# Kernel tuning notes

Hardware: AMD Instinct MI355X
Metric: run time of the kernel (lower is better)

## Reference

```python
import jax, jax.numpy as jnp
import numpy as np

B, L, H, D, T = 8, 4096, 8, 128, 128  # batch, max_len, kv_heads, head_size, max_new_tokens


def setup_inputs() -> dict:
    key = jax.random.key(0)
    ks = jax.random.split(key, 6)
    return {
        "keys": jax.random.normal(ks[0], (B, L, H, D), dtype=jnp.float32),
        "values": jax.random.normal(ks[1], (B, L, H, D), dtype=jnp.float32),
        "lengths": jax.random.randint(ks[2], (B,), 0, 2048, dtype=jnp.int32),
        "new_keys": jax.random.normal(ks[3], (B, T, H, D), dtype=jnp.float32),
        "new_values": jax.random.normal(ks[4], (B, T, H, D), dtype=jnp.float32),
        "new_lengths": jax.random.randint(ks[5], (B,), 0, T, dtype=jnp.int32),
    }


def reference(keys, values, lengths, new_keys, new_values, new_lengths):
    max_new_tokens = new_values.shape[1]
    max_len = keys.shape[1]
    operands = (keys, values, lengths, new_keys, new_values, new_lengths)

    def specialized_path(ops):
        k, v, l, nk, nv, nl = ops
        batch_size = k.shape[0]
        batch_idx = jnp.arange(batch_size)
        pos_idx = l
        update_vals_k = nk[:, 0]
        update_vals_v = nv[:, 0]
        should_update = (nl == 1)[:, None, None]
        original_vals_k = k[batch_idx, pos_idx]
        original_vals_v = v[batch_idx, pos_idx]
        vals_to_set_k = jnp.where(should_update, update_vals_k, original_vals_k)
        vals_to_set_v = jnp.where(should_update, update_vals_v, original_vals_v)
        updated_k = k.at[batch_idx, pos_idx].set(vals_to_set_k)
        updated_v = v.at[batch_idx, pos_idx].set(vals_to_set_v)
        return (updated_k, updated_v)

    def general_path(ops):
        k, v, l, nk, nv, nl = ops
        batch_size = k.shape[0]
        b_coords, p_coords = jnp.indices((batch_size, max_len))
        lengths_b = l[:, None]
        new_lengths_b = nl[:, None]
        update_mask = (p_coords >= lengths_b) & (p_coords < lengths_b + new_lengths_b)
        source_indices = p_coords - lengths_b
        clipped_source_indices = jnp.clip(source_indices, 0, max_new_tokens - 1)
        values_to_write_k = nk[b_coords, clipped_source_indices]
        values_to_write_v = nv[b_coords, clipped_source_indices]
        broadcast_mask = update_mask[:, :, None, None]
        updated_k = jnp.where(broadcast_mask, values_to_write_k, k)
        updated_v = jnp.where(broadcast_mask, values_to_write_v, v)
        return (updated_k, updated_v)

    is_special_case = jnp.all(new_lengths <= 1)
    updated_keys, updated_values = jax.lax.cond(is_special_case, specialized_path, general_path, operands)
    updated_lengths = lengths + new_lengths
    return (updated_keys, updated_values, updated_lengths)
```

## Files before the change

### kernel.cpp

```cpp
#include <hip/hip_runtime.h>

constexpr int B = 8;
constexpr int L = 4096;
constexpr int H = 8;
constexpr int D = 128;
constexpr int T = 128;

constexpr long long KV_ELEMS = (long long)B * L * H * D;
constexpr size_t KV_BYTES = (size_t)KV_ELEMS * sizeof(float);

__global__ __launch_bounds__(256) void kv_patch(
    const float4* __restrict__ new_keys,
    const float4* __restrict__ new_values,
    const int*    __restrict__ lengths,
    const int*    __restrict__ new_lengths,
    float4* __restrict__ out_k,
    float4* __restrict__ out_v,
    float*  __restrict__ out_len)
{
    const int b = blockIdx.x >> 7;
    const int t = blockIdx.x & (T - 1);

    if (t < new_lengths[b]) {
        const int l = lengths[b];
        const int c = threadIdx.x;
        const long long srci = ((long long)(b * T + t) << 8) + c;
        const long long dsti = ((long long)(b * L + l + t) << 8) + c;
        out_k[dsti] = new_keys[srci];
        out_v[dsti] = new_values[srci];
    }

    if (blockIdx.x == 0 && threadIdx.x < B) {
        const int bb = threadIdx.x;
        out_len[bb] = (float)(lengths[bb] + new_lengths[bb]);
    }
}

extern "C" void kernel_launch(void* const* d_in, const int* in_sizes, int n_in,
                              void* d_out, int out_size, void* d_ws, size_t ws_size,
                              hipStream_t stream)
{
    const void* keys        = d_in[0];
    const void* values      = d_in[1];
    const int*  lengths     = (const int*)d_in[2];
    const float4* new_keys  = (const float4*)d_in[3];
    const float4* new_values= (const float4*)d_in[4];
    const int*  new_lengths = (const int*)d_in[5];

    float*  out     = (float*)d_out;
    float4* out_k   = (float4*)out;
    float4* out_v   = (float4*)(out + KV_ELEMS);
    float*  out_len = out + 2 * KV_ELEMS;

    hipMemcpyAsync(out_k, keys,   KV_BYTES, hipMemcpyDeviceToDevice, stream);
    hipMemcpyAsync(out_v, values, KV_BYTES, hipMemcpyDeviceToDevice, stream);

    kv_patch<<<B * T, 256, 0, stream>>>(new_keys, new_values, lengths, new_lengths,
                                        out_k, out_v, out_len);
}
```

Measured before the change: 110.4 us.

## Fuse KV copy and patch into one nontemporal grid-stride kernel

Replaces two device-to-device memcpys plus a patch kernel with a single kernel that streams keys and values, substitutes new tokens in the update window, and writes outputs with nontemporal loads and stores. This is meant to remove the extra launches and the separate rewrite pass over patched rows. The loop is not unrolled and each thread keeps only one float4 per tensor in flight, which may limit memory parallelism compared with the tuned copy engine path.

```diff
diff --git a/kernel.cpp b/kernel.cpp
--- a/kernel.cpp
+++ b/kernel.cpp
@@ -7,27 +7,47 @@
 constexpr int T = 128;
 
 constexpr long long KV_ELEMS = (long long)B * L * H * D;
-constexpr size_t KV_BYTES = (size_t)KV_ELEMS * sizeof(float);
+constexpr int TOTAL4 = (int)(KV_ELEMS / 4);
 
-__global__ __launch_bounds__(256) void kv_patch(
-    const float4* __restrict__ new_keys,
-    const float4* __restrict__ new_values,
-    const int*    __restrict__ lengths,
-    const int*    __restrict__ new_lengths,
-    float4* __restrict__ out_k,
-    float4* __restrict__ out_v,
-    float*  __restrict__ out_len)
+constexpr int NBLOCKS = 2048;
+constexpr int NTHREADS = 256;
+constexpr int STRIDE = NBLOCKS * NTHREADS;
+
+typedef float f4 __attribute__((ext_vector_type(4)));
+
+__global__ __launch_bounds__(256) void kv_fused_nt(
+    const f4* __restrict__ keys,
+    const f4* __restrict__ values,
+    const int* __restrict__ lengths,
+    const f4* __restrict__ new_keys,
+    const f4* __restrict__ new_values,
+    const int* __restrict__ new_lengths,
+    f4* __restrict__ out_k,
+    f4* __restrict__ out_v,
+    float* __restrict__ out_len)
 {
-    const int b = blockIdx.x >> 7;
-    const int t = blockIdx.x & (T - 1);
+    int i = blockIdx.x * NTHREADS + (int)threadIdx.x;
 
-    if (t < new_lengths[b]) {
-        const int l = lengths[b];
-        const int c = threadIdx.x;
-        const long long srci = ((long long)(b * T + t) << 8) + c;
-        const long long dsti = ((long long)(b * L + l + t) << 8) + c;
-        out_k[dsti] = new_keys[srci];
-        out_v[dsti] = new_values[srci];
+    #pragma unroll 1
+    for (int it = 0; it < 16; ++it, i += STRIDE) {
+        f4 vk = __builtin_nontemporal_load(&keys[i]);
+        f4 vv = __builtin_nontemporal_load(&values[i]);
+
+        const int row = i >> 8;
+        const int b   = row >> 12;
+        const int p   = row & (L - 1);
+        const int l   = lengths[b];
+        const int nl  = new_lengths[b];
+
+        if (p >= l && p < l + nl) {
+            const int c    = i & 255;
+            const int nidx = ((b * T + (p - l)) << 8) + c;
+            vk = new_keys[nidx];
+            vv = new_values[nidx];
+        }
+
+        __builtin_nontemporal_store(vk, &out_k[i]);
+        __builtin_nontemporal_store(vv, &out_v[i]);
     }
 
     if (blockIdx.x == 0 && threadIdx.x < B) {
@@ -40,21 +60,19 @@
                               void* d_out, int out_size, void* d_ws, size_t ws_size,
                               hipStream_t stream)
 {
-    const void* keys        = d_in[0];
-    const void* values      = d_in[1];
-    const int*  lengths     = (const int*)d_in[2];
-    const float4* new_keys  = (const float4*)d_in[3];
-    const float4* new_values= (const float4*)d_in[4];
-    const int*  new_lengths = (const int*)d_in[5];
+    const f4* keys       = (const f4*)d_in[0];
+    const f4* values     = (const f4*)d_in[1];
+    const int* lengths   = (const int*)d_in[2];
+    const f4* new_keys   = (const f4*)d_in[3];
+    const f4* new_values = (const f4*)d_in[4];
+    const int* new_lengths = (const int*)d_in[5];
 
-    float*  out     = (float*)d_out;
-    float4* out_k   = (float4*)out;
-    float4* out_v   = (float4*)(out + KV_ELEMS);
-    float*  out_len = out + 2 * KV_ELEMS;
+    float* out   = (float*)d_out;
+    f4* out_k    = (f4*)out;
+    f4* out_v    = (f4*)(out + KV_ELEMS);
+    float* out_len = out + 2 * KV_ELEMS;
 
-    hipMemcpyAsync(out_k, keys,   KV_BYTES, hipMemcpyDeviceToDevice, stream);
-    hipMemcpyAsync(out_v, values, KV_BYTES, hipMemcpyDeviceToDevice, stream);
-
-    kv_patch<<<B * T, 256, 0, stream>>>(new_keys, new_values, lengths, new_lengths,
-                                        out_k, out_v, out_len);
+    kv_fused_nt<<<NBLOCKS, NTHREADS, 0, stream>>>(keys, values, lengths,
+                                                  new_keys, new_values, new_lengths,
+                                                  out_k, out_v, out_len);
 }
```

New measurement: 99.88 us. 9.5% less time.
